# Optimization experiments

Hardware: AMD Instinct MI355X
Metric: run time of the kernel (lower is better)

Reference implementation:

```python
import jax, jax.numpy as jnp
import numpy as np

W_ACTION_COUNT = 1.0
W_ACTION_TENSOR = 2.0


def setup_inputs() -> dict:
    key = jax.random.key(0)
    k1, k2, k3 = jax.random.split(key, 3)
    B, A, F = 4096, 2048, 8  # batch, max_actions, feature dim (axis-1 length = A + 1)
    predictions = jax.random.normal(k1, (B, A + 1, F), dtype=jnp.float32)
    targets = jax.random.normal(k2, (B, A + 1, F), dtype=jnp.float32)
    # Ground-truth action counts are integers stored as floats at [:, 0, 0].
    # Include zeros so the valid-batch filtering path is exercised.
    counts = jax.random.randint(k3, (B,), 0, A + 1).astype(jnp.float32)
    targets = targets.at[:, 0, 0].set(counts)
    return {"predictions": predictions, "targets": targets}


def reference(predictions, targets):
    # predictions/targets: (B, A+1, 8); index 0 along axis 1 carries the action count.
    pred_counts = predictions[:, 0, 0]            # (B,)
    target_counts = targets[:, 0, 0]              # (B,)
    pred_actions = predictions[:, 1:, :]          # (B, A, 8)
    target_actions = targets[:, 1:, :]            # (B, A, 8)

    count_loss = jnp.mean((pred_counts - target_counts) ** 2)

    A = pred_actions.shape[1]
    counts_int = target_counts.astype(jnp.int32)  # int(count.item()) truncation
    valid = counts_int > 0                        # (B,)
    mask = jnp.arange(A, dtype=jnp.int32)[None, :] < counts_int[:, None]  # (B, A)

    sq = (pred_actions - target_actions) ** 2     # (B, A, 8)
    per_sample_sum = jnp.sum(sq * mask[:, :, None].astype(sq.dtype), axis=(1, 2))  # (B,)
    denom = (counts_int * pred_actions.shape[2]).astype(sq.dtype)  # count * 8 elements
    per_sample_mse = jnp.where(valid, per_sample_sum / jnp.maximum(denom, 1.0), 0.0)

    n_valid = jnp.sum(valid.astype(sq.dtype))
    action_tensor_loss = jnp.sum(per_sample_mse) / jnp.maximum(n_valid, 1.0)

    total = W_ACTION_COUNT * count_loss + jnp.where(
        n_valid > 0, W_ACTION_TENSOR * action_tensor_loss, 0.0
    )
    return total
```

## Files before the change

kernel.cpp:

```cpp
#include <hip/hip_runtime.h>

#define NB    4096
#define AP1   2049
#define FEAT  8
#define ROWF  (AP1 * FEAT)


__global__ __launch_bounds__(256) void loss_main_kernel(
        const float* __restrict__ pred,
        const float* __restrict__ targ,
        float* __restrict__ ws) {
    const int b = blockIdx.x;
    const float* pb = pred + (size_t)b * ROWF;
    const float* tb = targ + (size_t)b * ROWF;

    const float tc = tb[0];
    const float pc = pb[0];
    const int count = (int)tc;

    const int nvec = count * 2;
    const float4* p4 = (const float4*)(pb + FEAT);
    const float4* t4 = (const float4*)(tb + FEAT);

    float s = 0.0f;
    int i = (int)threadIdx.x;
    const int stride = 256;

    for (; i + 3 * stride < nvec; i += 4 * stride) {
        const float4 a0 = p4[i];
        const float4 a1 = p4[i + stride];
        const float4 a2 = p4[i + 2 * stride];
        const float4 a3 = p4[i + 3 * stride];
        const float4 c0 = t4[i];
        const float4 c1 = t4[i + stride];
        const float4 c2 = t4[i + 2 * stride];
        const float4 c3 = t4[i + 3 * stride];
        float dx, dy, dz, dw;
        dx = a0.x - c0.x; dy = a0.y - c0.y; dz = a0.z - c0.z; dw = a0.w - c0.w;
        s += dx * dx + dy * dy + dz * dz + dw * dw;
        dx = a1.x - c1.x; dy = a1.y - c1.y; dz = a1.z - c1.z; dw = a1.w - c1.w;
        s += dx * dx + dy * dy + dz * dz + dw * dw;
        dx = a2.x - c2.x; dy = a2.y - c2.y; dz = a2.z - c2.z; dw = a2.w - c2.w;
        s += dx * dx + dy * dy + dz * dz + dw * dw;
        dx = a3.x - c3.x; dy = a3.y - c3.y; dz = a3.z - c3.z; dw = a3.w - c3.w;
        s += dx * dx + dy * dy + dz * dz + dw * dw;
    }
    for (; i < nvec; i += stride) {
        const float4 a = p4[i];
        const float4 c = t4[i];
        const float dx = a.x - c.x;
        const float dy = a.y - c.y;
        const float dz = a.z - c.z;
        const float dw = a.w - c.w;
        s += dx * dx + dy * dy + dz * dz + dw * dw;
    }

    #pragma unroll
    for (int o = 32; o > 0; o >>= 1) s += __shfl_down(s, o, 64);
    __shared__ float sm[4];
    const int wid  = threadIdx.x >> 6;
    const int lane = threadIdx.x & 63;
    if (lane == 0) sm[wid] = s;
    __syncthreads();

    if (threadIdx.x == 0) {
        const float total = sm[0] + sm[1] + sm[2] + sm[3];
        const float d = pc - tc;
        ws[b] = d * d;
        const bool valid = (count > 0);
        ws[NB + b]     = valid ? (total / (float)(count * FEAT)) : 0.0f;
        ws[2 * NB + b] = valid ? 1.0f : 0.0f;
    }
}

__global__ __launch_bounds__(256) void reduce_kernel(
        const float* __restrict__ ws, float* __restrict__ out) {
    float s0 = 0.0f, s1 = 0.0f, s2 = 0.0f;
    for (int i = threadIdx.x; i < NB; i += 256) {
        s0 += ws[i];
        s1 += ws[NB + i];
        s2 += ws[2 * NB + i];
    }
    #pragma unroll
    for (int o = 32; o > 0; o >>= 1) {
        s0 += __shfl_down(s0, o, 64);
        s1 += __shfl_down(s1, o, 64);
        s2 += __shfl_down(s2, o, 64);
    }
    __shared__ float sm[3][4];
    const int wid  = threadIdx.x >> 6;
    const int lane = threadIdx.x & 63;
    if (lane == 0) { sm[0][wid] = s0; sm[1][wid] = s1; sm[2][wid] = s2; }
    __syncthreads();
    if (threadIdx.x == 0) {
        const float count_sum = sm[0][0] + sm[0][1] + sm[0][2] + sm[0][3];
        const float mse_sum   = sm[1][0] + sm[1][1] + sm[1][2] + sm[1][3];
        const float nv        = sm[2][0] + sm[2][1] + sm[2][2] + sm[2][3];
        const float count_loss = count_sum * (1.0f / (float)NB);
        const float atl = (nv > 0.0f) ? (mse_sum / nv) : 0.0f;
        out[0] = count_loss + 2.0f * atl;
    }
}

extern "C" void kernel_launch(void* const* d_in, const int* in_sizes, int n_in,
                              void* d_out, int out_size, void* d_ws, size_t ws_size,
                              hipStream_t stream) {
    const float* pred = (const float*)d_in[0];
    const float* targ = (const float*)d_in[1];
    float* out = (float*)d_out;
    float* ws  = (float*)d_ws;

    loss_main_kernel<<<NB, 256, 0, stream>>>(pred, targ, ws);
    reduce_kernel<<<1, 256, 0, stream>>>(ws, out);
}
```

Baseline: 464.5 us.

## Fuse final reduction into main kernel via atomics and use nontemporal loads

Removes the separate single-block reduce kernel by accumulating per-sample results with global atomics and having the last-finishing block compute the final loss. It also switches the streaming loads to nontemporal vector loads to reduce cache pollution. It adds a memset launch and atomic contention on a few addresses, and makes the floating-point summation order nondeterministic.

```diff
diff --git a/kernel.cpp b/kernel.cpp
--- a/kernel.cpp
+++ b/kernel.cpp
@@ -5,11 +5,14 @@
 #define FEAT  8
 #define ROWF  (AP1 * FEAT)
 
+typedef float f32x4 __attribute__((ext_vector_type(4)));
 
-__global__ __launch_bounds__(256) void loss_main_kernel(
+
+__global__ __launch_bounds__(256) void loss_fused_kernel(
         const float* __restrict__ pred,
         const float* __restrict__ targ,
-        float* __restrict__ ws) {
+        float* __restrict__ ws,
+        float* __restrict__ out) {
     const int b = blockIdx.x;
     const float* pb = pred + (size_t)b * ROWF;
     const float* tb = targ + (size_t)b * ROWF;
@@ -19,40 +22,33 @@
     const int count = (int)tc;
 
     const int nvec = count * 2;
-    const float4* p4 = (const float4*)(pb + FEAT);
-    const float4* t4 = (const float4*)(tb + FEAT);
+    const f32x4* p4 = (const f32x4*)(pb + FEAT);
+    const f32x4* t4 = (const f32x4*)(tb + FEAT);
 
     float s = 0.0f;
     int i = (int)threadIdx.x;
     const int stride = 256;
 
     for (; i + 3 * stride < nvec; i += 4 * stride) {
-        const float4 a0 = p4[i];
-        const float4 a1 = p4[i + stride];
-        const float4 a2 = p4[i + 2 * stride];
-        const float4 a3 = p4[i + 3 * stride];
-        const float4 c0 = t4[i];
-        const float4 c1 = t4[i + stride];
-        const float4 c2 = t4[i + 2 * stride];
-        const float4 c3 = t4[i + 3 * stride];
-        float dx, dy, dz, dw;
-        dx = a0.x - c0.x; dy = a0.y - c0.y; dz = a0.z - c0.z; dw = a0.w - c0.w;
-        s += dx * dx + dy * dy + dz * dz + dw * dw;
-        dx = a1.x - c1.x; dy = a1.y - c1.y; dz = a1.z - c1.z; dw = a1.w - c1.w;
-        s += dx * dx + dy * dy + dz * dz + dw * dw;
-        dx = a2.x - c2.x; dy = a2.y - c2.y; dz = a2.z - c2.z; dw = a2.w - c2.w;
-        s += dx * dx + dy * dy + dz * dz + dw * dw;
-        dx = a3.x - c3.x; dy = a3.y - c3.y; dz = a3.z - c3.z; dw = a3.w - c3.w;
-        s += dx * dx + dy * dy + dz * dz + dw * dw;
+        const f32x4 a0 = __builtin_nontemporal_load(&p4[i]);
+        const f32x4 a1 = __builtin_nontemporal_load(&p4[i + stride]);
+        const f32x4 a2 = __builtin_nontemporal_load(&p4[i + 2 * stride]);
+        const f32x4 a3 = __builtin_nontemporal_load(&p4[i + 3 * stride]);
+        const f32x4 c0 = __builtin_nontemporal_load(&t4[i]);
+        const f32x4 c1 = __builtin_nontemporal_load(&t4[i + stride]);
+        const f32x4 c2 = __builtin_nontemporal_load(&t4[i + 2 * stride]);
+        const f32x4 c3 = __builtin_nontemporal_load(&t4[i + 3 * stride]);
+        f32x4 d;
+        d = a0 - c0; s += d.x * d.x + d.y * d.y + d.z * d.z + d.w * d.w;
+        d = a1 - c1; s += d.x * d.x + d.y * d.y + d.z * d.z + d.w * d.w;
+        d = a2 - c2; s += d.x * d.x + d.y * d.y + d.z * d.z + d.w * d.w;
+        d = a3 - c3; s += d.x * d.x + d.y * d.y + d.z * d.z + d.w * d.w;
     }
     for (; i < nvec; i += stride) {
-        const float4 a = p4[i];
-        const float4 c = t4[i];
-        const float dx = a.x - c.x;
-        const float dy = a.y - c.y;
-        const float dz = a.z - c.z;
-        const float dw = a.w - c.w;
-        s += dx * dx + dy * dy + dz * dz + dw * dw;
+        const f32x4 a = __builtin_nontemporal_load(&p4[i]);
+        const f32x4 c = __builtin_nontemporal_load(&t4[i]);
+        const f32x4 d = a - c;
+        s += d.x * d.x + d.y * d.y + d.z * d.z + d.w * d.w;
     }
 
     #pragma unroll
@@ -66,39 +62,23 @@
     if (threadIdx.x == 0) {
         const float total = sm[0] + sm[1] + sm[2] + sm[3];
         const float d = pc - tc;
-        ws[b] = d * d;
         const bool valid = (count > 0);
-        ws[NB + b]     = valid ? (total / (float)(count * FEAT)) : 0.0f;
-        ws[2 * NB + b] = valid ? 1.0f : 0.0f;
-    }
-}
 
-__global__ __launch_bounds__(256) void reduce_kernel(
-        const float* __restrict__ ws, float* __restrict__ out) {
-    float s0 = 0.0f, s1 = 0.0f, s2 = 0.0f;
-    for (int i = threadIdx.x; i < NB; i += 256) {
-        s0 += ws[i];
-        s1 += ws[NB + i];
-        s2 += ws[2 * NB + i];
-    }
-    #pragma unroll
-    for (int o = 32; o > 0; o >>= 1) {
-        s0 += __shfl_down(s0, o, 64);
-        s1 += __shfl_down(s1, o, 64);
-        s2 += __shfl_down(s2, o, 64);
-    }
-    __shared__ float sm[3][4];
-    const int wid  = threadIdx.x >> 6;
-    const int lane = threadIdx.x & 63;
-    if (lane == 0) { sm[0][wid] = s0; sm[1][wid] = s1; sm[2][wid] = s2; }
-    __syncthreads();
-    if (threadIdx.x == 0) {
-        const float count_sum = sm[0][0] + sm[0][1] + sm[0][2] + sm[0][3];
-        const float mse_sum   = sm[1][0] + sm[1][1] + sm[1][2] + sm[1][3];
-        const float nv        = sm[2][0] + sm[2][1] + sm[2][2] + sm[2][3];
-        const float count_loss = count_sum * (1.0f / (float)NB);
-        const float atl = (nv > 0.0f) ? (mse_sum / nv) : 0.0f;
-        out[0] = count_loss + 2.0f * atl;
+        atomicAdd(&ws[0], d * d);
+        if (valid) {
+            atomicAdd(&ws[1], total / (float)(count * FEAT));
+            atomicAdd(&ws[2], 1.0f);
+        }
+        __threadfence();
+        const unsigned old = atomicAdd((unsigned*)(ws + 3), 1u);
+        if (old == NB - 1) {
+            const float count_sum = atomicAdd(&ws[0], 0.0f);
+            const float mse_sum   = atomicAdd(&ws[1], 0.0f);
+            const float nv        = atomicAdd(&ws[2], 0.0f);
+            const float count_loss = count_sum * (1.0f / (float)NB);
+            const float atl = (nv > 0.0f) ? (mse_sum / nv) : 0.0f;
+            out[0] = count_loss + 2.0f * atl;
+        }
     }
 }
 
@@ -110,6 +90,6 @@
     float* out = (float*)d_out;
     float* ws  = (float*)d_ws;
 
-    loss_main_kernel<<<NB, 256, 0, stream>>>(pred, targ, ws);
-    reduce_kernel<<<1, 256, 0, stream>>>(ws, out);
+    (void)hipMemsetAsync(ws, 0, 16, stream);
+    loss_fused_kernel<<<NB, 256, 0, stream>>>(pred, targ, ws, out);
 }
```

After: 644.2 us. +38.7%, slower.
